# Kernel optimization log

Hardware: AMD Instinct MI355X
Metric: run time of the kernel (lower is better)

## Reference

```python
import jax, jax.numpy as jnp
import numpy as np

nA = 4096; nB = 4096; C = 128; H = 4; D = 32; E = 65536
EPS = 1e-5


def _ln(x, g, b):
    m = jnp.mean(x, axis=-1, keepdims=True)
    v = jnp.var(x, axis=-1, keepdims=True)
    return (x - m) / jnp.sqrt(v + EPS) * g + b


def setup_inputs() -> dict:
    key = jax.random.key(0)
    ks = jax.random.split(key, 16)
    w = 0.02
    inp = {}
    inp["x_a"] = jax.random.normal(ks[0], (nA, C), dtype=jnp.float32)
    inp["x_b"] = jax.random.normal(ks[1], (nB, C), dtype=jnp.float32)
    inp["edge_ab"] = jax.random.randint(ks[2], (2, E), 0, nA)  # row0: src in A, row1: dst in B
    inp["edge_ba"] = jax.random.randint(ks[3], (2, E), 0, nB)  # row0: src in B, row1: dst in A
    inp["Wq"] = jax.random.normal(ks[4], (C, C), dtype=jnp.float32) * w
    inp["bq"] = jnp.zeros((C,), jnp.float32)
    inp["Wk"] = jax.random.normal(ks[5], (C, C), dtype=jnp.float32) * w
    inp["bk"] = jnp.zeros((C,), jnp.float32)
    inp["Wv"] = jax.random.normal(ks[6], (C, C), dtype=jnp.float32) * w
    inp["bv"] = jnp.zeros((C,), jnp.float32)
    inp["Wo"] = jax.random.normal(ks[7], (C, C), dtype=jnp.float32) * w
    inp["bo"] = jnp.zeros((C,), jnp.float32)
    inp["g_attn"] = jnp.ones((C,), jnp.float32)   # pre_ln_attn
    inp["b_attn"] = jnp.zeros((C,), jnp.float32)
    inp["g_ffn"] = jnp.ones((C,), jnp.float32)    # pre_ln_ffn
    inp["b_ffn"] = jnp.zeros((C,), jnp.float32)
    inp["g_f"] = jnp.ones((C,), jnp.float32)      # LayerNorm inside ffn Sequential
    inp["b_f"] = jnp.zeros((C,), jnp.float32)
    inp["W1"] = jax.random.normal(ks[8], (C, C), dtype=jnp.float32) * w
    inp["b1"] = jnp.zeros((C,), jnp.float32)
    inp["W2"] = jax.random.normal(ks[9], (C, C), dtype=jnp.float32) * w
    inp["b2"] = jnp.zeros((C,), jnp.float32)
    inp["rel_ab"] = jax.random.normal(ks[10], (1,), dtype=jnp.float32)
    inp["rel_ba"] = jax.random.normal(ks[11], (1,), dtype=jnp.float32)
    return inp


def reference(x_a, x_b, edge_ab, edge_ba, Wq, bq, Wk, bk, Wv, bv, Wo, bo,
              g_attn, b_attn, g_ffn, b_ffn, g_f, b_f, W1, b1, W2, b2,
              rel_ab, rel_ba):
    inv_sqrt_d = 1.0 / jnp.sqrt(jnp.float32(D))

    def all_pairs_attn(xq, xkv, rel):
        nQ, nK = xq.shape[0], xkv.shape[0]
        Q = (xq @ Wq + bq).reshape(nQ, H, D)
        K = (xkv @ Wk + bk).reshape(nK, H, D)
        V = (xkv @ Wv + bv).reshape(nK, H, D)
        # [nQ, nK, H] logits with additive relation bias
        logits = jnp.einsum('ihd,jhd->ijh', Q, K) * inv_sqrt_d + rel
        a = jax.nn.softmax(logits, axis=1)  # softmax over all source nodes per dst
        return jnp.einsum('ijh,jhd->ihd', a, V).reshape(nQ, C)

    xn_a = _ln(x_a, g_attn, b_attn)
    xn_b = _ln(x_b, g_attn, b_attn)
    # edge type B->A contributes to dst type A; A->B to dst type B
    attn_a = all_pairs_attn(xn_a, xn_b, rel_ba[0]) @ Wo + bo
    attn_b = all_pairs_attn(xn_b, xn_a, rel_ab[0]) @ Wo + bo

    # total degree = out-degree + in-degree across edge types (eval: dropout = identity)
    ones = jnp.ones((E,), jnp.float32)
    deg_a = jax.ops.segment_sum(ones, edge_ab[0], num_segments=nA) + \
            jax.ops.segment_sum(ones, edge_ba[1], num_segments=nA)
    deg_b = jax.ops.segment_sum(ones, edge_ba[0], num_segments=nB) + \
            jax.ops.segment_sum(ones, edge_ab[1], num_segments=nB)
    attn_a = attn_a + deg_a[:, None]
    attn_b = attn_b + deg_b[:, None]

    res_a = x_a + attn_a
    res_b = x_b + attn_b

    def ffn(xr):
        h = _ln(xr, g_ffn, b_ffn)        # pre_ln_ffn
        h = _ln(h, g_f, b_f)             # LayerNorm inside ffn Sequential
        h = jax.nn.gelu(h @ W1 + b1, approximate=False)
        return h @ W2 + b2

    out_a = res_a + ffn(res_a)
    out_b = res_b + ffn(res_b)
    return jnp.stack([out_a, out_b])  # [2, n, C]
```

## Files before the change

### kernel.cpp

```cpp
#include <hip/hip_runtime.h>

typedef unsigned short u16;
typedef unsigned int   u32;
typedef __attribute__((ext_vector_type(8))) short bf16x8;
typedef __attribute__((ext_vector_type(4))) float f32x4;

#define NEL (8192*128)

#define ASYNC16(ldsptr, gptr) __builtin_amdgcn_global_load_lds( \
    (const __attribute__((address_space(1))) u32*)(gptr), \
    (__attribute__((address_space(3))) u32*)(ldsptr), 16, 0, 0)

__device__ __forceinline__ u16 f2bf(float f){
  u32 u = __builtin_bit_cast(u32, f);
  u = (u + 0x7FFFu + ((u >> 16) & 1u)) >> 16;
  return (u16)u;
}
__device__ __forceinline__ u32 pk2(float a, float b){
  u32 r;
  asm("v_cvt_pk_bf16_f32 %0, %1, %2" : "=v"(r) : "v"(a), "v"(b));
  return r;
}

__global__ __launch_bounds__(256) void prep_kernel(
    const int* __restrict__ eab, const int* __restrict__ eba, float* __restrict__ deg,
    const float* __restrict__ Wq, const float* __restrict__ Wk, const float* __restrict__ Wv,
    const float* __restrict__ Wo, const float* __restrict__ W1, const float* __restrict__ W2,
    u16* __restrict__ WT)
{
  __shared__ float tile[32][33];
  const int b = blockIdx.x, t = threadIdx.x;
  if (b < 256){
    int e = b*256 + t;
    atomicAdd(&deg[eab[e]],              1.f);
    atomicAdd(&deg[4096 + eab[65536+e]], 1.f);
    atomicAdd(&deg[4096 + eba[e]],       1.f);
    atomicAdd(&deg[eba[65536+e]],        1.f);
  } else {
    int id = b - 256;
    int w = id >> 4, tt = id & 15, tr = tt >> 2, tc = tt & 3;
    const float* W = (w==0)?Wq:(w==1)?Wk:(w==2)?Wv:(w==3)?Wo:(w==4)?W1:W2;
    int r = t >> 3, c4 = (t&7)*4;
    float4 v = *(const float4*)(W + (tr*32 + r)*128 + tc*32 + c4);
    tile[r][c4]=v.x; tile[r][c4+1]=v.y; tile[r][c4+2]=v.z; tile[r][c4+3]=v.w;
    __syncthreads();
    int n = t >> 3, k4 = (t&7)*4;
    u32 lo = pk2(tile[k4+0][n], tile[k4+1][n]);
    u32 hi = pk2(tile[k4+2][n], tile[k4+3][n]);
    *(uint2*)(WT + w*16384 + (tc*32+n)*128 + tr*32 + k4) = make_uint2(lo, hi);
  }
}

__global__ __launch_bounds__(512) void ln_qkv_kernel(
    const float* __restrict__ xa, const float* __restrict__ xb,
    const float* __restrict__ g, const float* __restrict__ bvec,
    const u16* __restrict__ WT,
    const float* __restrict__ bq, const float* __restrict__ bk, const float* __restrict__ bv,
    u16* __restrict__ Qb, u16* __restrict__ Kb, u16* __restrict__ VT)
{
  __shared__ float xs[16][132];
  __shared__ __align__(16) u16 abf[16][128];
  __shared__ __align__(16) u16 vtb[128][24];
  const int t = threadIdx.x, lane = t&63, wave = t>>6;
  const int lq = lane&15, lg = lane>>4;
  const int row0 = blockIdx.x*16;
  const float* x = (row0 < 4096) ? (xa + row0*128) : (xb + (row0-4096)*128);
  {
    int r = t>>5, c4 = (t&31)*4;
    float4 v = *(const float4*)(x + r*128 + c4);
    xs[r][c4]=v.x; xs[r][c4+1]=v.y; xs[r][c4+2]=v.z; xs[r][c4+3]=v.w;
  }
  __syncthreads();
  if (t < 256){
    int r = t>>4, c0 = t&15;
    float s=0.f, s2=0.f;
    #pragma unroll
    for (int j=0;j<8;j++){ float v = xs[r][c0+j*16]; s+=v; s2+=v*v; }
    #pragma unroll
    for (int m=1;m<16;m<<=1){ s += __shfl_xor(s,m); s2 += __shfl_xor(s2,m); }
    float mean = s*0.0078125f;
    float var  = s2*0.0078125f - mean*mean;
    float rstd = rsqrtf(var + 1e-5f);
    #pragma unroll
    for (int j=0;j<8;j++){
      int c = c0 + j*16;
      float h = (xs[r][c]-mean)*rstd*g[c] + bvec[c];
      int sj = (c>>3) ^ (r&7);
      abf[r][sj*8 + (c&7)] = f2bf(h);
    }
  }
  __syncthreads();
  bf16x8 af[4];
  #pragma unroll
  for (int s=0;s<4;s++){
    int sj = (s*4+lg) ^ (lq&7);
    af[s] = *(const bf16x8*)&abf[lq][sj*8];
  }
  const int cb = wave*16;
  const float QSC = 0.17677669529663687f * 1.4426950408889634f;
  #pragma unroll
  for (int m=0;m<3;m++){
    const u16* Wg = WT + m*16384;
    bf16x8 bfr[4];
    #pragma unroll
    for (int s=0;s<4;s++)
      bfr[s] = *(const bf16x8*)(Wg + (cb+lq)*128 + s*32 + lg*8);
    f32x4 acc = {0,0,0,0};
    #pragma unroll
    for (int s=0;s<4;s++)
      acc = __builtin_amdgcn_mfma_f32_16x16x32_bf16(af[s], bfr[s], acc, 0,0,0);
    int col = cb + lq;
    if (m==0){
      float bb = bq[col];
      #pragma unroll
      for (int r=0;r<4;r++)
        Qb[(row0+4*lg+r)*128 + col] = f2bf((acc[r]+bb)*QSC);
    } else if (m==1){
      float bb = bk[col];
      #pragma unroll
      for (int r=0;r<4;r++)
        Kb[(row0+4*lg+r)*128 + col] = f2bf(acc[r]+bb);
    } else {
      float bb = bv[col];
      #pragma unroll
      for (int r=0;r<4;r++)
        vtb[col][4*lg+r] = f2bf(acc[r]+bb);
    }
  }
  __syncthreads();
  if (t < 256){
    int c = t>>1, half = t&1;
    bf16x8 v = *(const bf16x8*)&vtb[c][half*8];
    *(bf16x8*)(VT + c*8192 + row0 + half*8) = v;
  }
}

__global__ __launch_bounds__(256) void attn_kernel(
    const u16* __restrict__ Qb, const u16* __restrict__ Kb,
    const u16* __restrict__ VT, float* __restrict__ numb, float* __restrict__ denb)
{
  __shared__ __align__(16) u16 Klds[2][2048];
  __shared__ __align__(16) u16 Vlds[2][2048];
  __shared__ __align__(16) u16 Plds[4][1024];
  const int t = threadIdx.x, wave = t>>6, lane = t&63;
  const int lq = lane&15, lg = lane>>4;
  const int h = blockIdx.y;
  const int dir = blockIdx.z >> 2, sp = blockIdx.z & 3;
  const int q = blockIdx.x*64 + wave*16 + lq + (dir ? 4096 : 0);
  const int kvb = (dir ? 0 : 4096) + sp*1024;

  bf16x8 qf = *(const bf16x8*)(Qb + q*128 + h*32 + lg*8);
  f32x4 acc0 = {0,0,0,0}, acc1 = {0,0,0,0}, accL = {0,0,0,0};
  bf16x8 ones;
  #pragma unroll
  for (int i=0;i<8;i++) ones[i] = (short)0x3F80;

  const u16* gk = Kb + (kvb + (t>>2))*128 + h*32 + ((t&3) ^ ((t>>3)&3))*8;
  const u16* gv = VT + (h*32 + (t>>3))*8192 + kvb + ((t&7) ^ ((t>>3)&7))*8;

  ASYNC16(&Klds[0][t*8], gk);
  ASYNC16(&Vlds[0][t*8], gv);
  asm volatile("s_waitcnt vmcnt(0)" ::: "memory");
  __builtin_amdgcn_s_barrier();

  int cur = 0;
  for (int kt=0; kt<16; ++kt){
    if (kt < 15){
      gk += 8192; gv += 64;
      ASYNC16(&Klds[cur^1][t*8], gk);
      ASYNC16(&Vlds[cur^1][t*8], gv);
    }
    const u16* KL = Klds[cur];
    const u16* VL = Vlds[cur];
    u16* PL = Plds[wave] + lq*64;
    const int ksj = lg ^ ((lq>>1)&3);
    #pragma unroll
    for (int f=0; f<4; ++f){
      bf16x8 kf = *(const bf16x8*)(KL + (f*16+lq)*32 + ksj*8);
      f32x4 st = __builtin_amdgcn_mfma_f32_16x16x32_bf16(kf, qf, (f32x4){0.f,0.f,0.f,0.f}, 0,0,0);
      float p0 = __builtin_amdgcn_exp2f(st[0]);
      float p1 = __builtin_amdgcn_exp2f(st[1]);
      float p2 = __builtin_amdgcn_exp2f(st[2]);
      float p3 = __builtin_amdgcn_exp2f(st[3]);
      int j = f*2 + (lg>>1);
      *(uint2*)(PL + ((j ^ (lq&7))<<3) + (lg&1)*4) = make_uint2(pk2(p0,p1), pk2(p2,p3));
    }
    #pragma unroll
    for (int kc=0; kc<2; ++kc){
      int sj = (kc*4+lg) ^ (lq&7);
      bf16x8 pf  = *(const bf16x8*)(PL + (sj<<3));
      bf16x8 vf0 = *(const bf16x8*)(VL + lq*64      + (sj<<3));
      bf16x8 vf1 = *(const bf16x8*)(VL + (16+lq)*64 + (sj<<3));
      acc0 = __builtin_amdgcn_mfma_f32_16x16x32_bf16(vf0,  pf, acc0, 0,0,0);
      acc1 = __builtin_amdgcn_mfma_f32_16x16x32_bf16(vf1,  pf, acc1, 0,0,0);
      accL = __builtin_amdgcn_mfma_f32_16x16x32_bf16(ones, pf, accL, 0,0,0);
    }
    asm volatile("s_waitcnt vmcnt(0)" ::: "memory");
    __builtin_amdgcn_s_barrier();
    cur ^= 1;
  }
  float* outp = numb + sp*NEL + q*128 + h*32 + 4*lg;
  *(float4*)(outp)      = make_float4(acc0[0], acc0[1], acc0[2], acc0[3]);
  *(float4*)(outp + 16) = make_float4(acc1[0], acc1[1], acc1[2], acc1[3]);
  if (lg == 0) denb[sp*32768 + q*4 + h] = accL[0];
}

__global__ __launch_bounds__(512) void tail_kernel(
    const float* __restrict__ numb, const float* __restrict__ denb,
    const u16* __restrict__ WT,
    const float* __restrict__ bo, const float* __restrict__ deg,
    const float* __restrict__ xa, const float* __restrict__ xb,
    const float* __restrict__ gf1, const float* __restrict__ bf1,
    const float* __restrict__ gf2, const float* __restrict__ bf2,
    const float* __restrict__ b1, const float* __restrict__ b2,
    float* __restrict__ out)
{
  __shared__ __align__(16) u16 abf[16][128];
  __shared__ float rs[16][132];
  const int t = threadIdx.x, lane = t&63, wave = t>>6;
  const int lq = lane&15, lg = lane>>4;
  const int row0 = blockIdx.x*16;
  const int cb = wave*16;

  {
    int r = t>>5, c0 = (t&31)*4, hh = c0>>5;
    const float* np = numb + (row0+r)*128 + c0;
    float4 s0 = *(const float4*)(np);
    float4 s1 = *(const float4*)(np + NEL);
    float4 s2 = *(const float4*)(np + 2*NEL);
    float4 s3 = *(const float4*)(np + 3*NEL);
    int di = (row0+r)*4 + hh;
    float den = denb[di] + denb[32768+di] + denb[65536+di] + denb[98304+di];
    float inv = 1.0f/den;
    float a0 = (s0.x+s1.x+s2.x+s3.x)*inv;
    float a1 = (s0.y+s1.y+s2.y+s3.y)*inv;
    float a2 = (s0.z+s1.z+s2.z+s3.z)*inv;
    float a3 = (s0.w+s1.w+s2.w+s3.w)*inv;
    int sj = (c0>>3) ^ (r&7);
    *(uint2*)&abf[r][sj*8 + (c0&7)] = make_uint2(pk2(a0,a1), pk2(a2,a3));
  }
  __syncthreads();

  bf16x8 af[4];
  #pragma unroll
  for (int s=0;s<4;s++){ int sj = (s*4+lg) ^ (lq&7); af[s] = *(const bf16x8*)&abf[lq][sj*8]; }

  f32x4 acc = {0,0,0,0};
  {
    const u16* Wg = WT + 3*16384;
    bf16x8 bfr[4];
    #pragma unroll
    for (int s=0;s<4;s++) bfr[s] = *(const bf16x8*)(Wg + (cb+lq)*128 + s*32 + lg*8);
    #pragma unroll
    for (int s=0;s<4;s++) acc = __builtin_amdgcn_mfma_f32_16x16x32_bf16(af[s], bfr[s], acc, 0,0,0);
  }
  const float* xres = (row0<4096)? (xa + row0*128) : (xb + (row0-4096)*128);
  const int col = cb + lq;
  float rv[4];
  {
    float bb = bo[col];
    #pragma unroll
    for (int r=0;r<4;r++){
      int lr = 4*lg + r;
      rv[r] = acc[r] + bb + deg[row0+lr] + xres[lr*128 + col];
      rs[lr][col] = rv[r];
    }
  }
  __syncthreads();
  if (t < 256){
    int r = t>>4, c0 = t&15;
    float s=0.f, s2=0.f;
    #pragma unroll
    for (int j=0;j<8;j++){ float v = rs[r][c0+j*16]; s+=v; s2+=v*v; }
    #pragma unroll
    for (int m=1;m<16;m<<=1){ s += __shfl_xor(s,m); s2 += __shfl_xor(s2,m); }
    float mean = s*0.0078125f;
    float var  = s2*0.0078125f - mean*mean;
    float rstd = rsqrtf(var + 1e-5f);
    float h8[8];
    #pragma unroll
    for (int j=0;j<8;j++){ int c=c0+j*16; h8[j] = (rs[r][c]-mean)*rstd*gf1[c] + bf1[c]; }
    s=0.f; s2=0.f;
    #pragma unroll
    for (int j=0;j<8;j++){ s+=h8[j]; s2+=h8[j]*h8[j]; }
    #pragma unroll
    for (int m=1;m<16;m<<=1){ s += __shfl_xor(s,m); s2 += __shfl_xor(s2,m); }
    float mean2 = s*0.0078125f;
    float var2  = s2*0.0078125f - mean2*mean2;
    float rstd2 = rsqrtf(var2 + 1e-5f);
    #pragma unroll
    for (int j=0;j<8;j++){
      int c = c0 + j*16;
      float h = (h8[j]-mean2)*rstd2*gf2[c] + bf2[c];
      int sj = (c>>3) ^ (r&7);
      abf[r][sj*8 + (c&7)] = f2bf(h);
    }
  }
  __syncthreads();
  #pragma unroll
  for (int s=0;s<4;s++){ int sj = (s*4+lg) ^ (lq&7); af[s] = *(const bf16x8*)&abf[lq][sj*8]; }
  acc = (f32x4){0,0,0,0};
  {
    const u16* Wg = WT + 4*16384;
    bf16x8 bfr[4];
    #pragma unroll
    for (int s=0;s<4;s++) bfr[s] = *(const bf16x8*)(Wg + (cb+lq)*128 + s*32 + lg*8);
    #pragma unroll
    for (int s=0;s<4;s++) acc = __builtin_amdgcn_mfma_f32_16x16x32_bf16(af[s], bfr[s], acc, 0,0,0);
  }
  float gvv[4];
  {
    float bb = b1[col];
    #pragma unroll
    for (int r=0;r<4;r++){
      float v = acc[r] + bb;
      gvv[r] = 0.5f*v*(1.f + erff(v*0.70710678118654752f));
    }
  }
  __syncthreads();
  #pragma unroll
  for (int r=0;r<4;r++){
    int lr = 4*lg + r;
    int sj = (col>>3) ^ (lr&7);
    abf[lr][sj*8 + (col&7)] = f2bf(gvv[r]);
  }
  __syncthreads();
  #pragma unroll
  for (int s=0;s<4;s++){ int sj = (s*4+lg) ^ (lq&7); af[s] = *(const bf16x8*)&abf[lq][sj*8]; }
  acc = (f32x4){0,0,0,0};
  {
    const u16* Wg = WT + 5*16384;
    bf16x8 bfr[4];
    #pragma unroll
    for (int s=0;s<4;s++) bfr[s] = *(const bf16x8*)(Wg + (cb+lq)*128 + s*32 + lg*8);
    #pragma unroll
    for (int s=0;s<4;s++) acc = __builtin_amdgcn_mfma_f32_16x16x32_bf16(af[s], bfr[s], acc, 0,0,0);
  }
  {
    float bb = b2[col];
    #pragma unroll
    for (int r=0;r<4;r++){
      int lr = 4*lg + r;
      out[(row0+lr)*128 + col] = acc[r] + bb + rv[r];
    }
  }
}

extern "C" void kernel_launch(void* const* d_in, const int* in_sizes, int n_in,
                              void* d_out, int out_size, void* d_ws, size_t ws_size,
                              hipStream_t stream) {
  const float* xa  = (const float*)d_in[0];
  const float* xb  = (const float*)d_in[1];
  const int*   eab = (const int*)d_in[2];
  const int*   eba = (const int*)d_in[3];
  const float* Wq  = (const float*)d_in[4];   const float* bq = (const float*)d_in[5];
  const float* Wk  = (const float*)d_in[6];   const float* bk = (const float*)d_in[7];
  const float* Wv  = (const float*)d_in[8];   const float* bv = (const float*)d_in[9];
  const float* Wo  = (const float*)d_in[10];  const float* bo = (const float*)d_in[11];
  const float* ga  = (const float*)d_in[12];  const float* ba = (const float*)d_in[13];
  const float* gfn = (const float*)d_in[14];  const float* bfn= (const float*)d_in[15];
  const float* gf  = (const float*)d_in[16];  const float* bf = (const float*)d_in[17];
  const float* W1  = (const float*)d_in[18];  const float* b1 = (const float*)d_in[19];
  const float* W2  = (const float*)d_in[20];  const float* b2 = (const float*)d_in[21];
  float* out = (float*)d_out;

  char* w = (char*)d_ws;
  float* deg  = (float*)w;
  u16*   WT   = (u16*)(w + 32768);
  u16*   Qb   = (u16*)(w + 32768 + 196608);
  u16*   Kb   = Qb + NEL;
  u16*   VT   = Kb + NEL;
  float* numb = (float*)(VT + NEL);
  float* denb = numb + 4*NEL;

  hipMemsetAsync(deg, 0, 8192*sizeof(float), stream);
  prep_kernel<<<352, 256, 0, stream>>>(eab, eba, deg, Wq, Wk, Wv, Wo, W1, W2, WT);
  ln_qkv_kernel<<<512, 512, 0, stream>>>(xa, xb, ga, ba, WT, bq, bk, bv, Qb, Kb, VT);
  attn_kernel<<<dim3(64,4,8), 256, 0, stream>>>(Qb, Kb, VT, numb, denb);
  tail_kernel<<<512, 512, 0, stream>>>(numb, denb, WT, bo, deg, xa, xb,
                                       gfn, bfn, gf, bf, b1, b2, out);
}
```

Baseline: 184.3 us.

## Replace global degree atomics with per-block LDS histograms and fused reduction

The degree count now uses a 32 KB shared-memory histogram in each of 64 blocks instead of global float atomics, and each block writes its histogram as a partial array. The 64 partials are summed in the first 32 blocks of the LN/QKV kernel, so the memset launch is no longer needed. This is meant to cut global atomic contention and one launch. In exchange it adds 2 MB of partial writes and reads, reuses the numb buffer as scratch, and gives those 32 blocks of the LN/QKV kernel a serial 64-term sum to do.

```diff
diff --git a/kernel.cpp b/kernel.cpp
--- a/kernel.cpp
+++ b/kernel.cpp
@@ -23,21 +23,35 @@
 }
 
 __global__ __launch_bounds__(256) void prep_kernel(
-    const int* __restrict__ eab, const int* __restrict__ eba, float* __restrict__ deg,
+    const int* __restrict__ eab, const int* __restrict__ eba, float* __restrict__ partial,
     const float* __restrict__ Wq, const float* __restrict__ Wk, const float* __restrict__ Wv,
     const float* __restrict__ Wo, const float* __restrict__ W1, const float* __restrict__ W2,
     u16* __restrict__ WT)
 {
+  __shared__ u32 hist[8192];
   __shared__ float tile[32][33];
   const int b = blockIdx.x, t = threadIdx.x;
-  if (b < 256){
-    int e = b*256 + t;
-    atomicAdd(&deg[eab[e]],              1.f);
-    atomicAdd(&deg[4096 + eab[65536+e]], 1.f);
-    atomicAdd(&deg[4096 + eba[e]],       1.f);
-    atomicAdd(&deg[eba[65536+e]],        1.f);
+  if (b < 64){
+    #pragma unroll
+    for (int i=0;i<32;i++) hist[t + i*256] = 0u;
+    __syncthreads();
+    const int e0 = b*1024;
+    #pragma unroll
+    for (int i=0;i<4;i++){
+      int e = e0 + t + i*256;
+      atomicAdd(&hist[eab[e]],              1u);
+      atomicAdd(&hist[4096 + eab[65536+e]], 1u);
+      atomicAdd(&hist[4096 + eba[e]],       1u);
+      atomicAdd(&hist[eba[65536+e]],        1u);
+    }
+    __syncthreads();
+    #pragma unroll
+    for (int i=0;i<32;i++){
+      int bin = t + i*256;
+      partial[b*8192 + bin] = (float)hist[bin];
+    }
   } else {
-    int id = b - 256;
+    int id = b - 64;
     int w = id >> 4, tt = id & 15, tr = tt >> 2, tc = tt & 3;
     const float* W = (w==0)?Wq:(w==1)?Wk:(w==2)?Wv:(w==3)?Wo:(w==4)?W1:W2;
     int r = t >> 3, c4 = (t&7)*4;
@@ -56,6 +70,7 @@
     const float* __restrict__ g, const float* __restrict__ bvec,
     const u16* __restrict__ WT,
     const float* __restrict__ bq, const float* __restrict__ bk, const float* __restrict__ bv,
+    const float* __restrict__ partial, float* __restrict__ deg,
     u16* __restrict__ Qb, u16* __restrict__ Kb, u16* __restrict__ VT)
 {
   __shared__ float xs[16][132];
@@ -133,6 +148,13 @@
     bf16x8 v = *(const bf16x8*)&vtb[c][half*8];
     *(bf16x8*)(VT + c*8192 + row0 + half*8) = v;
   }
+  if (blockIdx.x < 32 && t < 256){
+    int bin = blockIdx.x*256 + t;
+    float s = 0.f;
+    #pragma unroll
+    for (int j=0;j<64;j++) s += partial[j*8192 + bin];
+    deg[bin] = s;
+  }
 }
 
 __global__ __launch_bounds__(256) void attn_kernel(
@@ -372,10 +394,11 @@
   u16*   VT   = Kb + NEL;
   float* numb = (float*)(VT + NEL);
   float* denb = numb + 4*NEL;
-
-  hipMemsetAsync(deg, 0, 8192*sizeof(float), stream);
-  prep_kernel<<<352, 256, 0, stream>>>(eab, eba, deg, Wq, Wk, Wv, Wo, W1, W2, WT);
-  ln_qkv_kernel<<<512, 512, 0, stream>>>(xa, xb, ga, ba, WT, bq, bk, bv, Qb, Kb, VT);
+  float* partial = numb;
+
+  prep_kernel<<<160, 256, 0, stream>>>(eab, eba, partial, Wq, Wk, Wv, Wo, W1, W2, WT);
+  ln_qkv_kernel<<<512, 512, 0, stream>>>(xa, xb, ga, ba, WT, bq, bk, bv,
+                                         partial, deg, Qb, Kb, VT);
   attn_kernel<<<dim3(64,4,8), 256, 0, stream>>>(Qb, Kb, VT, numb, denb);
   tail_kernel<<<512, 512, 0, stream>>>(numb, denb, WT, bo, deg, xa, xb,
                                        gfn, bfn, gf, bf, b1, b2, out);
```

After: 184.5 us. No clear change (+0.1%).
